# Kernel tuning notes

Measured on AMD Instinct MI355X. Metric: run time of the kernel, lower is better.

## Reference

```python
import jax, jax.numpy as jnp
import numpy as np

B, S, K = 4, 512, 16              # batch, seq_len, random-walk PE length (positional_size)
VOCAB = 50265
D_EMB = 768 - 16 + 16             # 768 - positional_size + extra_positional_size
D_CAT = D_EMB + K                 # 784 = 768 + extra_positional_size


def setup_inputs() -> dict:
    key = jax.random.key(0)
    k0, k1, k2, k3, k4 = jax.random.split(key, 5)
    code_inputs = jax.random.randint(k0, (B, S), 0, VOCAB)
    position_idx = jax.random.randint(k1, (B, S), 0, 8)
    attn_mask = jax.random.randint(k2, (B, S, S), 0, 2).astype(bool)
    emb_table = jax.random.normal(k3, (VOCAB, D_EMB), dtype=jnp.float32) * 0.02
    w_lin = jax.random.normal(k4, (D_CAT, VOCAB), dtype=jnp.float32) * 0.02
    b_lin = jnp.zeros((VOCAB,), dtype=jnp.float32)
    return {"code_inputs": code_inputs, "position_idx": position_idx,
            "attn_mask": attn_mask, "emb_table": emb_table,
            "w_lin": w_lin, "b_lin": b_lin}


def random_walk_pe(attn_mask):
    # adjacency = attn_mask with forced self-loops (adj[:, a, a] = 1)
    eye = jnp.eye(S, dtype=bool)
    A = jnp.where(eye[None], 1.0, attn_mask.astype(jnp.float32))   # [B,S,S]
    deg = A.sum(-1)                                                # out-degree (row sum)
    inv_deg = jnp.where(deg > 0, 1.0 / deg, 0.0)
    M = A * inv_deg[:, :, None]                                    # RW transition D^-1 A

    def step(P, _):
        Pn = jnp.einsum('bij,bjk->bik', P, M)
        return Pn, jnp.diagonal(Pn, axis1=1, axis2=2)              # diag of M^i

    P0 = jnp.broadcast_to(jnp.eye(S, dtype=jnp.float32), (B, S, S))
    _, diags = jax.lax.scan(step, P0, None, length=K)              # [K,B,S]
    return jnp.moveaxis(diags, 0, -1)                              # [B,S,K]


def reference(code_inputs, position_idx, attn_mask, emb_table, w_lin, b_lin):
    nodes_mask = position_idx == 0        # [B,S] DFG nodes
    token_mask = position_idx >= 2        # [B,S] code tokens

    emb = emb_table[code_inputs]          # [B,S,D_EMB]

    # masked average of token embeddings into node positions
    ntm = (nodes_mask[:, :, None] & token_mask[:, None, :] & attn_mask).astype(jnp.float32)
    ntm = ntm / (ntm.sum(-1, keepdims=True) + 1e-10)
    avg = jnp.einsum('abc,acd->abd', ntm, emb)
    emb = jnp.where(nodes_mask[:, :, None], avg, emb)

    pe = random_walk_pe(attn_mask)                    # [B,S,K]
    x = jnp.concatenate([emb, pe], axis=-1)           # [B,S,D_CAT]

    # (external pretrained BERT encoder omitted — identity; see notes)
    logit = jnp.einsum('bsd,dv->bsv', x, w_lin) + b_lin
    return logit
```

## Files before the change

### kernel.cpp

```cpp
#include <hip/hip_runtime.h>

#define VOCAB_N 50265
#define NPAD    50304
#define KX      832
#define DEMB    768
#define DCAT    784
#define SEQ     512
#define NBATCH  4
#define OUT_ROWS 2048
#define PE_ELE  ((size_t)NBATCH*SEQ*SEQ)

typedef unsigned short u16;
typedef unsigned long long u64;
typedef short s16x8 __attribute__((ext_vector_type(8)));
typedef float f32x4 __attribute__((ext_vector_type(4)));
typedef u16   u16x4 __attribute__((ext_vector_type(4)));

#define AS1 __attribute__((address_space(1)))
#define AS3 __attribute__((address_space(3)))

__device__ __forceinline__ u16 f2bf(float f){
  unsigned u = __builtin_bit_cast(unsigned, f);
  u = (u + 0x7FFFu + ((u >> 16) & 1u)) >> 16;
  return (u16)u;
}
__device__ __forceinline__ float bf2f(u16 h){
  return __builtin_bit_cast(float, (unsigned)h << 16);
}
__device__ __forceinline__ void gl_lds16(const void* g, void* l){
  __builtin_amdgcn_global_load_lds((const AS1 unsigned*)g, (AS3 unsigned*)l, 16, 0, 0);
}
__device__ __forceinline__ int xcd_remap(int bid, int nwg){
  int q = nwg >> 3, r = nwg & 7;
  int xc = bid & 7, i = bid >> 3;
  int base = xc < r ? xc*(q+1) : r*(q+1) + (xc - r)*q;
  return base + i;
}

__global__ __launch_bounds__(256) void wconv(const float* __restrict__ w, u16* __restrict__ wT){
  __shared__ float tile[64][65];
  const int n0 = blockIdx.x * 64;
  const int k0 = blockIdx.y * 64;
  const int t = threadIdx.x;
#pragma unroll
  for (int i = 0; i < 16; ++i){
    int idx = t + i*256;
    int kk = idx >> 6, nn = idx & 63;
    int k = k0 + kk, n = n0 + nn;
    float v = 0.f;
    if (k < DCAT && n < VOCAB_N) v = w[(size_t)k*VOCAB_N + n];
    tile[kk][nn] = v;
  }
  __syncthreads();
#pragma unroll
  for (int i = 0; i < 4; ++i){
    int idx = t + i*256;
    int nn = idx >> 4, ks = (idx & 15) * 4;
    u16x4 o;
    o[0] = f2bf(tile[ks+0][nn]);
    o[1] = f2bf(tile[ks+1][nn]);
    o[2] = f2bf(tile[ks+2][nn]);
    o[3] = f2bf(tile[ks+3][nn]);
    *reinterpret_cast<u16x4*>(&wT[(size_t)(n0+nn)*KX + k0 + ks]) = o;
  }
}

__global__ __launch_bounds__(256) void gather_emb(const int* __restrict__ code, const float* __restrict__ emb,
                                                  u16* __restrict__ x){
  const int row = blockIdx.x;
  const int c = code[row];
  const float* e = emb + (size_t)c * DEMB;
  for (int i = threadIdx.x; i < KX; i += 256){
    u16 v = 0;
    if (i < DEMB) v = f2bf(e[i]);
    x[(size_t)row*KX + i] = v;
  }
}

__global__ __launch_bounds__(256) void node_avg(const int* __restrict__ code, const int* __restrict__ pos,
                                                const int* __restrict__ attn, const float* __restrict__ emb,
                                                u16* __restrict__ x){
  const int row = blockIdx.x;
  const int b = row >> 9, i = row & (SEQ-1);
  if (pos[row] != 0) return;
  __shared__ unsigned char sel[SEQ];
  __shared__ int crow[SEQ];
  __shared__ int cnt_s;
  const int t = threadIdx.x;
  if (t == 0) cnt_s = 0;
  __syncthreads();
  int local = 0;
  for (int j = t; j < SEQ; j += 256){
    bool s = (pos[b*SEQ + j] >= 2) && (attn[((size_t)(b*SEQ + i))*SEQ + j] != 0);
    sel[j] = s ? 1 : 0;
    crow[j] = code[b*SEQ + j];
    local += s ? 1 : 0;
  }
  atomicAdd(&cnt_s, local);
  __syncthreads();
  const float scale = 1.0f / ((float)cnt_s + 1e-10f);
  for (int d = t; d < DEMB; d += 256){
    float acc = 0.f;
    for (int j = 0; j < SEQ; ++j){
      if (sel[j]) acc += emb[(size_t)crow[j]*DEMB + d];
    }
    x[(size_t)row*KX + d] = f2bf(acc * scale);
  }
}

__global__ __launch_bounds__(256) void build_M(const int* __restrict__ attn, u16* __restrict__ M,
                                               u16* __restrict__ MT, u16* __restrict__ x){
  const int row = blockIdx.x;
  const int b = row >> 9, i = row & (SEQ-1);
  __shared__ float arow[SEQ];
  __shared__ int deg_s;
  const int t = threadIdx.x;
  if (t == 0) deg_s = 0;
  __syncthreads();
  int local = 0;
  for (int j = t; j < SEQ; j += 256){
    int a = (j == i) ? 1 : ((attn[((size_t)(b*SEQ + i))*SEQ + j] != 0) ? 1 : 0);
    arow[j] = (float)a;
    local += a;
  }
  atomicAdd(&deg_s, local);
  __syncthreads();
  const float inv = 1.0f / (float)deg_s;
  for (int j = t; j < SEQ; j += 256){
    u16 m = f2bf(arow[j] * inv);
    M [((size_t)(b*SEQ + i))*SEQ + j] = m;
    MT[((size_t)(b*SEQ + j))*SEQ + i] = m;
  }
  if (t == 0) x[(size_t)row*KX + DEMB] = f2bf(inv);
}

__global__ __launch_bounds__(256) void pe_pow(const u16* __restrict__ A, const u16* __restrict__ Bn,
                                              u16* __restrict__ C, u16* __restrict__ x, int xcol){
  const int m0 = blockIdx.x * 64, n0 = blockIdx.y * 64, b = blockIdx.z;
  const u16* Ab = A  + (size_t)b*SEQ*SEQ;
  const u16* Bb = Bn + (size_t)b*SEQ*SEQ;
  __shared__ __align__(16) u16 Al[64*64];
  __shared__ __align__(16) u16 Bl[64*64];
  const int t = threadIdx.x, lane = t & 63, w = t >> 6;
  const int wr = w >> 1, wc = w & 1;
  f32x4 acc[2][2] = {};
  const int srow = lane >> 3;
  const int scol = ((lane & 7) ^ srow) * 8;
  for (int k0 = 0; k0 < SEQ; k0 += 64){
    __syncthreads();
#pragma unroll
    for (int c = 0; c < 2; ++c){
      int chunk = w*2 + c;
      int r = chunk*8 + srow;
      gl_lds16(Ab + (size_t)(m0 + r)*SEQ + k0 + scol, Al + chunk*512);
      gl_lds16(Bb + (size_t)(n0 + r)*SEQ + k0 + scol, Bl + chunk*512);
    }
    asm volatile("s_waitcnt vmcnt(0)" ::: "memory");
    __syncthreads();
#pragma unroll
    for (int kin = 0; kin < 2; ++kin){
      s16x8 fa[2], fb[2];
      const int kb = kin*64 + (lane >> 4)*16;
#pragma unroll
      for (int m = 0; m < 2; ++m){
        int r = wr*32 + m*16 + (lane & 15);
        fa[m] = *reinterpret_cast<const s16x8*>((const char*)Al + r*128 + (kb ^ ((r & 7) << 4)));
      }
#pragma unroll
      for (int n = 0; n < 2; ++n){
        int r = wc*32 + n*16 + (lane & 15);
        fb[n] = *reinterpret_cast<const s16x8*>((const char*)Bl + r*128 + (kb ^ ((r & 7) << 4)));
      }
#pragma unroll
      for (int m = 0; m < 2; ++m)
#pragma unroll
        for (int n = 0; n < 2; ++n)
          acc[m][n] = __builtin_amdgcn_mfma_f32_16x16x32_bf16(fa[m], fb[n], acc[m][n], 0, 0, 0);
    }
  }
#pragma unroll
  for (int m = 0; m < 2; ++m)
#pragma unroll
   for (int n = 0; n < 2; ++n)
#pragma unroll
    for (int r = 0; r < 4; ++r){
      int gm = m0 + wr*32 + m*16 + (lane >> 4)*4 + r;
      int gn = n0 + wc*32 + n*16 + (lane & 15);
      u16 bv = f2bf(acc[m][n][r]);
      C[((size_t)(b*SEQ + gm))*SEQ + gn] = bv;
      if (gm == gn) x[(size_t)(b*SEQ + gm)*KX + xcol] = bv;
    }
}

__global__ __launch_bounds__(256) void transpose_k(const u16* __restrict__ in, u16* __restrict__ outp){
  const int i0 = blockIdx.x*64, j0 = blockIdx.y*64, b = blockIdx.z;
  const u16* ib = in   + (size_t)b*SEQ*SEQ;
  u16*       ob = outp + (size_t)b*SEQ*SEQ;
  __shared__ u16 tile[64][66];
  const int t = threadIdx.x;
#pragma unroll
  for (int it = 0; it < 2; ++it){
    int jj = it*32 + (t >> 3), ii = (t & 7)*8;
    s16x8 v = *reinterpret_cast<const s16x8*>(ib + (size_t)(j0+jj)*SEQ + i0 + ii);
#pragma unroll
    for (int q = 0; q < 8; ++q) tile[jj][ii+q] = (u16)v[q];
  }
  __syncthreads();
#pragma unroll
  for (int it = 0; it < 2; ++it){
    int ii = it*32 + (t >> 3), jj8 = (t & 7)*8;
    u16 tmp[8];
#pragma unroll
    for (int q = 0; q < 8; ++q) tmp[q] = tile[jj8+q][ii];
    *reinterpret_cast<s16x8*>(ob + (size_t)(i0+ii)*SEQ + j0 + jj8) = *reinterpret_cast<s16x8*>(tmp);
  }
}

__global__ __launch_bounds__(256) void pe_dots(const u16* __restrict__ M, const u16* __restrict__ pw,
                                               const u16* __restrict__ p8t, u16* __restrict__ x){
  const int row = blockIdx.x;
  const int lane = threadIdx.x & 63, w = threadIdx.x >> 6;
  const u16* t8 = p8t + (size_t)row*SEQ;
  s16x8 vb = *reinterpret_cast<const s16x8*>(t8 + lane*8);
#pragma unroll
  for (int s = 0; s < 2; ++s){
    int a = 1 + w + s*4;
    const u16* Pa = (a == 1) ? (M + (size_t)row*SEQ) : (pw + (size_t)(a-2)*PE_ELE + (size_t)row*SEQ);
    s16x8 va = *reinterpret_cast<const s16x8*>(Pa + lane*8);
    float acc = 0.f;
#pragma unroll
    for (int q = 0; q < 8; ++q) acc += bf2f((u16)va[q]) * bf2f((u16)vb[q]);
#pragma unroll
    for (int m = 32; m; m >>= 1) acc += __shfl_xor(acc, m, 64);
    if (lane == 0) x[(size_t)row*KX + DEMB + 8 + (a-1)] = f2bf(acc);
  }
}

__global__ __launch_bounds__(256) void gemm_fast(const u16* __restrict__ X, const u16* __restrict__ WT,
                                                 const float* __restrict__ bias, float* __restrict__ out,
                                                 int nmt, int nwg){
  const int lid = xcd_remap(blockIdx.x, nwg);
  const int mt = lid % nmt, nt = lid / nmt;
  const int m0 = mt*128, n0 = nt*128;
  __shared__ __align__(16) u16 Al[128*64];
  __shared__ __align__(16) u16 Bl[128*64];
  const int t = threadIdx.x, lane = t & 63, w = t >> 6;
  const int wr = w >> 1, wc = w & 1;
  f32x4 acc[4][4] = {};
  const int srow = lane >> 3;
  const int scol = ((lane & 7) ^ srow) * 8;
  for (int k0 = 0; k0 < KX; k0 += 64){
    __syncthreads();
#pragma unroll
    for (int c = 0; c < 4; ++c){
      int chunk = w*4 + c;
      int r = chunk*8 + srow;
      gl_lds16(X  + (size_t)(m0 + r)*KX + k0 + scol, Al + chunk*512);
      gl_lds16(WT + (size_t)(n0 + r)*KX + k0 + scol, Bl + chunk*512);
    }
    asm volatile("s_waitcnt vmcnt(0)" ::: "memory");
    __syncthreads();
#pragma unroll
    for (int kin = 0; kin < 2; ++kin){
      s16x8 fa[4], fb[4];
      const int kb = kin*64 + (lane >> 4)*16;
#pragma unroll
      for (int m = 0; m < 4; ++m){
        int r = wr*64 + m*16 + (lane & 15);
        fa[m] = *reinterpret_cast<const s16x8*>((const char*)Al + r*128 + (kb ^ ((r & 7) << 4)));
      }
#pragma unroll
      for (int n = 0; n < 4; ++n){
        int r = wc*64 + n*16 + (lane & 15);
        fb[n] = *reinterpret_cast<const s16x8*>((const char*)Bl + r*128 + (kb ^ ((r & 7) << 4)));
      }
#pragma unroll
      for (int m = 0; m < 4; ++m)
#pragma unroll
        for (int n = 0; n < 4; ++n)
          acc[m][n] = __builtin_amdgcn_mfma_f32_16x16x32_bf16(fa[m], fb[n], acc[m][n], 0, 0, 0);
    }
  }
#pragma unroll
  for (int m = 0; m < 4; ++m)
#pragma unroll
   for (int n = 0; n < 4; ++n)
#pragma unroll
    for (int r = 0; r < 4; ++r){
      int gm = m0 + wr*64 + m*16 + (lane >> 4)*4 + r;
      int gn = n0 + wc*64 + n*16 + (lane & 15);
      if (gn < VOCAB_N)
        out[(size_t)gm*VOCAB_N + gn] = acc[m][n][r] + bias[gn];
    }
}

__global__ __launch_bounds__(256) void gemm_slow(const u16* __restrict__ X, const float* __restrict__ W,
                                                 const float* __restrict__ bias, float* __restrict__ out,
                                                 int nwg){
  const int lid = xcd_remap(blockIdx.x, nwg);
  const int mt = 12 + (lid & 3), nt = lid >> 2;
  const int m0 = mt*128, n0 = nt*128;
  __shared__ __align__(16) u16 Al[128*64];
  __shared__ __align__(16) u16 Bl[128*64];
  char* Blc = reinterpret_cast<char*>(Bl);
  const int t = threadIdx.x, lane = t & 63, w = t >> 6;
  const int wr = w >> 1, wc = w & 1;
  f32x4 acc[4][4] = {};
  const int srow = lane >> 3;
  const int scol = ((lane & 7) ^ srow) * 8;
  const int nn  = t & 127;
  const int kk0 = (t >> 7) * 32;
  const int ng  = n0 + nn;
  const bool nok = (ng < VOCAB_N);
  const int bsw = nn*128;
  const int xsw = (nn & 15) << 3;
  for (int k0 = 0; k0 < KX; k0 += 64){
    __syncthreads();
#pragma unroll
    for (int c = 0; c < 4; ++c){
      int chunk = w*4 + c;
      int r = chunk*8 + srow;
      gl_lds16(X + (size_t)(m0 + r)*KX + k0 + scol, Al + chunk*512);
    }
#pragma unroll
    for (int i = 0; i < 16; ++i){
      int k = kk0 + 2*i;
      int gk = k0 + k;
      float f0 = (nok && gk     < DCAT) ? W[(size_t)gk    *VOCAB_N + ng] : 0.f;
      float f1 = (nok && gk + 1 < DCAT) ? W[(size_t)(gk+1)*VOCAB_N + ng] : 0.f;
      unsigned pk = (unsigned)f2bf(f0) | ((unsigned)f2bf(f1) << 16);
      *reinterpret_cast<unsigned*>(Blc + bsw + ((k*2) ^ xsw)) = pk;
    }
    asm volatile("s_waitcnt vmcnt(0)" ::: "memory");
    __syncthreads();
#pragma unroll
    for (int kin = 0; kin < 2; ++kin){
      s16x8 fa[4], fb[4];
      const int kb = kin*64 + (lane >> 4)*16;
#pragma unroll
      for (int m = 0; m < 4; ++m){
        int r = wr*64 + m*16 + (lane & 15);
        fa[m] = *reinterpret_cast<const s16x8*>((const char*)Al + r*128 + (kb ^ ((r & 7) << 4)));
      }
#pragma unroll
      for (int n = 0; n < 4; ++n){
        int row = wc*64 + n*16 + (lane & 15);
        int kbb = kin*64 + (lane >> 4)*16;
        int rsw = (row & 15) << 3;
        u64 h0 = *reinterpret_cast<const u64*>(Blc + row*128 + ((kbb    ) ^ rsw));
        u64 h1 = *reinterpret_cast<const u64*>(Blc + row*128 + ((kbb + 8) ^ rsw));
        struct U128 { u64 a, b; } u{h0, h1};
        fb[n] = __builtin_bit_cast(s16x8, u);
      }
#pragma unroll
      for (int m = 0; m < 4; ++m)
#pragma unroll
        for (int n = 0; n < 4; ++n)
          acc[m][n] = __builtin_amdgcn_mfma_f32_16x16x32_bf16(fa[m], fb[n], acc[m][n], 0, 0, 0);
    }
  }
#pragma unroll
  for (int m = 0; m < 4; ++m)
#pragma unroll
   for (int n = 0; n < 4; ++n)
#pragma unroll
    for (int r = 0; r < 4; ++r){
      int gm = m0 + wr*64 + m*16 + (lane >> 4)*4 + r;
      int gn = n0 + wc*64 + n*16 + (lane & 15);
      if (gn < VOCAB_N)
        out[(size_t)gm*VOCAB_N + gn] = acc[m][n][r] + bias[gn];
    }
}

extern "C" void kernel_launch(void* const* d_in, const int* in_sizes, int n_in,
                              void* d_out, int out_size, void* d_ws, size_t ws_size,
                              hipStream_t stream) {
  (void)in_sizes; (void)n_in; (void)out_size;
  const int*   code = (const int*)d_in[0];
  const int*   pos  = (const int*)d_in[1];
  const int*   attn = (const int*)d_in[2];
  const float* emb  = (const float*)d_in[3];
  const float* wlin = (const float*)d_in[4];
  const float* bias = (const float*)d_in[5];
  float* out = (float*)d_out;

  const size_t WT_ELE  = (size_t)NPAD * KX;
  const size_t X_ELE   = (size_t)OUT_ROWS * KX;
  const size_t OUT_ELE = (size_t)OUT_ROWS * VOCAB_N;
  const size_t need_full = (WT_ELE + X_ELE + 2*PE_ELE + 8*PE_ELE) * sizeof(u16);

  u16 *wT, *x, *M, *MT, *pw, *p8t;
  const bool compact = (ws_size < need_full);
  if (!compact){
    wT  = (u16*)d_ws;
    x   = wT + WT_ELE;
    M   = x  + X_ELE;
    MT  = M  + PE_ELE;
    pw  = MT + PE_ELE;
    p8t = pw + 7*PE_ELE;
  } else {
    x   = (u16*)d_ws;
    M   = x + X_ELE;
    MT  = M + PE_ELE;
    pw  = (u16*)d_out;
    p8t = pw + 7*PE_ELE;
    wT  = (u16*)d_out + (OUT_ELE*2 - WT_ELE);
  }

  wconv     <<<dim3(NPAD/64, KX/64), 256, 0, stream>>>(wlin, wT);
  gather_emb<<<NBATCH*SEQ, 256, 0, stream>>>(code, emb, x);
  node_avg  <<<NBATCH*SEQ, 256, 0, stream>>>(code, pos, attn, emb, x);
  build_M   <<<NBATCH*SEQ, 256, 0, stream>>>(attn, M, MT, x);

  const u16* A = M;
  for (int c = 2; c <= 8; ++c){
    u16* C = pw + (size_t)(c-2)*PE_ELE;
    pe_pow<<<dim3(8,8,NBATCH), 256, 0, stream>>>(A, MT, C, x, DEMB + (c-1));
    A = C;
  }
  transpose_k<<<dim3(8,8,NBATCH), 256, 0, stream>>>(pw + 6*PE_ELE, p8t);
  pe_dots<<<NBATCH*SEQ, 256, 0, stream>>>(M, pw, p8t, x);

  if (!compact){
    const int nwg = (NPAD/128)*16;
    gemm_fast<<<nwg, 256, 0, stream>>>(x, wT, bias, out, 16, nwg);
  } else {
    const int nwg_f = (NPAD/128)*12;
    gemm_fast<<<nwg_f, 256, 0, stream>>>(x, wT, bias, out, 12, nwg_f);
    const int nwg_s = (NPAD/128)*4;
    gemm_slow<<<nwg_s, 256, 0, stream>>>(x, wlin, bias, out, nwg_s);
  }
}
```

Baseline: 1.151 ms.

## Double-buffer LDS in GEMMs, compact node_avg gather list, tiled transpose for MT

The main logits GEMM and the PE power GEMM now use two LDS buffers, so the global-to-LDS loads for the next k tile are issued before the MFMAs on the current tile run, hiding load latency. node_avg builds a compact list of selected token rows with an atomic counter and accumulates them with float4 loads, instead of scanning all 512 positions per column. build_M no longer writes the transpose with strided scattered stores; a tiled transpose kernel produces MT instead. Double buffering doubles LDS use per block, which may lower occupancy, and the atomic list makes the summation order in node_avg nondeterministic.

```diff
diff --git a/kernel.cpp b/kernel.cpp
--- a/kernel.cpp
+++ b/kernel.cpp
@@ -81,39 +81,47 @@
                                                 const int* __restrict__ attn, const float* __restrict__ emb,
                                                 u16* __restrict__ x){
   const int row = blockIdx.x;
-  const int b = row >> 9, i = row & (SEQ-1);
+  const int b = row >> 9;
   if (pos[row] != 0) return;
-  __shared__ unsigned char sel[SEQ];
-  __shared__ int crow[SEQ];
+  __shared__ int list[SEQ];
   __shared__ int cnt_s;
   const int t = threadIdx.x;
   if (t == 0) cnt_s = 0;
   __syncthreads();
-  int local = 0;
   for (int j = t; j < SEQ; j += 256){
-    bool s = (pos[b*SEQ + j] >= 2) && (attn[((size_t)(b*SEQ + i))*SEQ + j] != 0);
-    sel[j] = s ? 1 : 0;
-    crow[j] = code[b*SEQ + j];
-    local += s ? 1 : 0;
-  }
-  atomicAdd(&cnt_s, local);
-  __syncthreads();
-  const float scale = 1.0f / ((float)cnt_s + 1e-10f);
-  for (int d = t; d < DEMB; d += 256){
-    float acc = 0.f;
-    for (int j = 0; j < SEQ; ++j){
-      if (sel[j]) acc += emb[(size_t)crow[j]*DEMB + d];
-    }
-    x[(size_t)row*KX + d] = f2bf(acc * scale);
+    if (pos[b*SEQ + j] >= 2 && attn[(size_t)row*SEQ + j] != 0){
+      int slot = atomicAdd(&cnt_s, 1);
+      list[slot] = code[b*SEQ + j] * DEMB;
+    }
+  }
+  __syncthreads();
+  const int cnt = cnt_s;
+  const float scale = 1.0f / ((float)cnt + 1e-10f);
+  if (t < DEMB/4){
+    f32x4 acc = {};
+    int k = 0;
+    for (; k + 4 <= cnt; k += 4){
+      f32x4 v0 = reinterpret_cast<const f32x4*>(emb + list[k+0])[t];
+      f32x4 v1 = reinterpret_cast<const f32x4*>(emb + list[k+1])[t];
+      f32x4 v2 = reinterpret_cast<const f32x4*>(emb + list[k+2])[t];
+      f32x4 v3 = reinterpret_cast<const f32x4*>(emb + list[k+3])[t];
+      acc += v0; acc += v1; acc += v2; acc += v3;
+    }
+    for (; k < cnt; ++k)
+      acc += reinterpret_cast<const f32x4*>(emb + list[k])[t];
+    u16x4 o;
+#pragma unroll
+    for (int q = 0; q < 4; ++q) o[q] = f2bf(acc[q] * scale);
+    *reinterpret_cast<u16x4*>(&x[(size_t)row*KX + t*4]) = o;
   }
 }
 
 __global__ __launch_bounds__(256) void build_M(const int* __restrict__ attn, u16* __restrict__ M,
-                                               u16* __restrict__ MT, u16* __restrict__ x){
+                                               u16* __restrict__ x){
   const int row = blockIdx.x;
   const int b = row >> 9, i = row & (SEQ-1);
+  __shared__ int deg_s;
   __shared__ float arow[SEQ];
-  __shared__ int deg_s;
   const int t = threadIdx.x;
   if (t == 0) deg_s = 0;
   __syncthreads();
@@ -126,37 +134,59 @@
   atomicAdd(&deg_s, local);
   __syncthreads();
   const float inv = 1.0f / (float)deg_s;
-  for (int j = t; j < SEQ; j += 256){
-    u16 m = f2bf(arow[j] * inv);
-    M [((size_t)(b*SEQ + i))*SEQ + j] = m;
-    MT[((size_t)(b*SEQ + j))*SEQ + i] = m;
-  }
+  for (int j = t; j < SEQ; j += 256)
+    M[((size_t)(b*SEQ + i))*SEQ + j] = f2bf(arow[j] * inv);
   if (t == 0) x[(size_t)row*KX + DEMB] = f2bf(inv);
 }
+
+__global__ __launch_bounds__(256) void transpose_k(const u16* __restrict__ in, u16* __restrict__ outp){
+  const int i0 = blockIdx.x*64, j0 = blockIdx.y*64, b = blockIdx.z;
+  const u16* ib = in   + (size_t)b*SEQ*SEQ;
+  u16*       ob = outp + (size_t)b*SEQ*SEQ;
+  __shared__ u16 tile[64][66];
+  const int t = threadIdx.x;
+#pragma unroll
+  for (int it = 0; it < 2; ++it){
+    int jj = it*32 + (t >> 3), ii = (t & 7)*8;
+    s16x8 v = *reinterpret_cast<const s16x8*>(ib + (size_t)(j0+jj)*SEQ + i0 + ii);
+#pragma unroll
+    for (int q = 0; q < 8; ++q) tile[jj][ii+q] = (u16)v[q];
+  }
+  __syncthreads();
+#pragma unroll
+  for (int it = 0; it < 2; ++it){
+    int ii = it*32 + (t >> 3), jj8 = (t & 7)*8;
+    u16 tmp[8];
+#pragma unroll
+    for (int q = 0; q < 8; ++q) tmp[q] = tile[jj8+q][ii];
+    *reinterpret_cast<s16x8*>(ob + (size_t)(i0+ii)*SEQ + j0 + jj8) = *reinterpret_cast<s16x8*>(tmp);
+  }
+}
+
+#define PP_STAGE(kt, bf) do{ const int _k0 = (kt)*64;                              \
+  for (int _c = 0; _c < 2; ++_c){                                                  \
+    int _ch = w*2 + _c; int _r = _ch*8 + srow;                                     \
+    gl_lds16(Ab + (size_t)(m0 + _r)*SEQ + _k0 + scol, &Al[bf][_ch*512]);           \
+    gl_lds16(Bb + (size_t)(n0 + _r)*SEQ + _k0 + scol, &Bl[bf][_ch*512]); } }while(0)
 
 __global__ __launch_bounds__(256) void pe_pow(const u16* __restrict__ A, const u16* __restrict__ Bn,
                                               u16* __restrict__ C, u16* __restrict__ x, int xcol){
   const int m0 = blockIdx.x * 64, n0 = blockIdx.y * 64, b = blockIdx.z;
   const u16* Ab = A  + (size_t)b*SEQ*SEQ;
   const u16* Bb = Bn + (size_t)b*SEQ*SEQ;
-  __shared__ __align__(16) u16 Al[64*64];
-  __shared__ __align__(16) u16 Bl[64*64];
+  __shared__ __align__(16) u16 Al[2][64*64];
+  __shared__ __align__(16) u16 Bl[2][64*64];
   const int t = threadIdx.x, lane = t & 63, w = t >> 6;
   const int wr = w >> 1, wc = w & 1;
   f32x4 acc[2][2] = {};
   const int srow = lane >> 3;
   const int scol = ((lane & 7) ^ srow) * 8;
-  for (int k0 = 0; k0 < SEQ; k0 += 64){
-    __syncthreads();
-#pragma unroll
-    for (int c = 0; c < 2; ++c){
-      int chunk = w*2 + c;
-      int r = chunk*8 + srow;
-      gl_lds16(Ab + (size_t)(m0 + r)*SEQ + k0 + scol, Al + chunk*512);
-      gl_lds16(Bb + (size_t)(n0 + r)*SEQ + k0 + scol, Bl + chunk*512);
-    }
-    asm volatile("s_waitcnt vmcnt(0)" ::: "memory");
-    __syncthreads();
+  PP_STAGE(0, 0);
+  asm volatile("s_waitcnt vmcnt(0)" ::: "memory");
+  __syncthreads();
+  for (int kt = 0; kt < SEQ/64; ++kt){
+    const int cur = kt & 1;
+    if (kt + 1 < SEQ/64) PP_STAGE(kt+1, cur^1);
 #pragma unroll
     for (int kin = 0; kin < 2; ++kin){
       s16x8 fa[2], fb[2];
@@ -164,12 +194,12 @@
 #pragma unroll
       for (int m = 0; m < 2; ++m){
         int r = wr*32 + m*16 + (lane & 15);
-        fa[m] = *reinterpret_cast<const s16x8*>((const char*)Al + r*128 + (kb ^ ((r & 7) << 4)));
+        fa[m] = *reinterpret_cast<const s16x8*>((const char*)&Al[cur][0] + r*128 + (kb ^ ((r & 7) << 4)));
       }
 #pragma unroll
       for (int n = 0; n < 2; ++n){
         int r = wc*32 + n*16 + (lane & 15);
-        fb[n] = *reinterpret_cast<const s16x8*>((const char*)Bl + r*128 + (kb ^ ((r & 7) << 4)));
+        fb[n] = *reinterpret_cast<const s16x8*>((const char*)&Bl[cur][0] + r*128 + (kb ^ ((r & 7) << 4)));
       }
 #pragma unroll
       for (int m = 0; m < 2; ++m)
@@ -177,6 +207,8 @@
         for (int n = 0; n < 2; ++n)
           acc[m][n] = __builtin_amdgcn_mfma_f32_16x16x32_bf16(fa[m], fb[n], acc[m][n], 0, 0, 0);
     }
+    asm volatile("s_waitcnt vmcnt(0)" ::: "memory");
+    __syncthreads();
   }
 #pragma unroll
   for (int m = 0; m < 2; ++m)
@@ -192,30 +224,6 @@
     }
 }
 
-__global__ __launch_bounds__(256) void transpose_k(const u16* __restrict__ in, u16* __restrict__ outp){
-  const int i0 = blockIdx.x*64, j0 = blockIdx.y*64, b = blockIdx.z;
-  const u16* ib = in   + (size_t)b*SEQ*SEQ;
-  u16*       ob = outp + (size_t)b*SEQ*SEQ;
-  __shared__ u16 tile[64][66];
-  const int t = threadIdx.x;
-#pragma unroll
-  for (int it = 0; it < 2; ++it){
-    int jj = it*32 + (t >> 3), ii = (t & 7)*8;
-    s16x8 v = *reinterpret_cast<const s16x8*>(ib + (size_t)(j0+jj)*SEQ + i0 + ii);
-#pragma unroll
-    for (int q = 0; q < 8; ++q) tile[jj][ii+q] = (u16)v[q];
-  }
-  __syncthreads();
-#pragma unroll
-  for (int it = 0; it < 2; ++it){
-    int ii = it*32 + (t >> 3), jj8 = (t & 7)*8;
-    u16 tmp[8];
-#pragma unroll
-    for (int q = 0; q < 8; ++q) tmp[q] = tile[jj8+q][ii];
-    *reinterpret_cast<s16x8*>(ob + (size_t)(i0+ii)*SEQ + j0 + jj8) = *reinterpret_cast<s16x8*>(tmp);
-  }
-}
-
 __global__ __launch_bounds__(256) void pe_dots(const u16* __restrict__ M, const u16* __restrict__ pw,
                                                const u16* __restrict__ p8t, u16* __restrict__ x){
   const int row = blockIdx.x;
@@ -236,30 +244,32 @@
   }
 }
 
+#define GF_STAGE(kt, bf) do{ const int _k0 = (kt)*64;                              \
+  for (int _c = 0; _c < 4; ++_c){                                                  \
+    int _ch = w*4 + _c; int _r = _ch*8 + srow;                                     \
+    gl_lds16(X  + (size_t)(m0 + _r)*KX + _k0 + scol, &Al[bf][_ch*512]);            \
+    gl_lds16(WT + (size_t)(n0 + _r)*KX + _k0 + scol, &Bl[bf][_ch*512]); } }while(0)
+
 __global__ __launch_bounds__(256) void gemm_fast(const u16* __restrict__ X, const u16* __restrict__ WT,
                                                  const float* __restrict__ bias, float* __restrict__ out,
                                                  int nmt, int nwg){
   const int lid = xcd_remap(blockIdx.x, nwg);
   const int mt = lid % nmt, nt = lid / nmt;
   const int m0 = mt*128, n0 = nt*128;
-  __shared__ __align__(16) u16 Al[128*64];
-  __shared__ __align__(16) u16 Bl[128*64];
+  __shared__ __align__(16) u16 Al[2][128*64];
+  __shared__ __align__(16) u16 Bl[2][128*64];
   const int t = threadIdx.x, lane = t & 63, w = t >> 6;
   const int wr = w >> 1, wc = w & 1;
   f32x4 acc[4][4] = {};
   const int srow = lane >> 3;
   const int scol = ((lane & 7) ^ srow) * 8;
-  for (int k0 = 0; k0 < KX; k0 += 64){
-    __syncthreads();
-#pragma unroll
-    for (int c = 0; c < 4; ++c){
-      int chunk = w*4 + c;
-      int r = chunk*8 + srow;
-      gl_lds16(X  + (size_t)(m0 + r)*KX + k0 + scol, Al + chunk*512);
-      gl_lds16(WT + (size_t)(n0 + r)*KX + k0 + scol, Bl + chunk*512);
-    }
-    asm volatile("s_waitcnt vmcnt(0)" ::: "memory");
-    __syncthreads();
+  GF_STAGE(0, 0);
+  asm volatile("s_waitcnt vmcnt(0)" ::: "memory");
+  __syncthreads();
+  const int NKT = KX/64;
+  for (int kt = 0; kt < NKT; ++kt){
+    const int cur = kt & 1;
+    if (kt + 1 < NKT) GF_STAGE(kt+1, cur^1);
 #pragma unroll
     for (int kin = 0; kin < 2; ++kin){
       s16x8 fa[4], fb[4];
@@ -267,12 +277,12 @@
 #pragma unroll
       for (int m = 0; m < 4; ++m){
         int r = wr*64 + m*16 + (lane & 15);
-        fa[m] = *reinterpret_cast<const s16x8*>((const char*)Al + r*128 + (kb ^ ((r & 7) << 4)));
+        fa[m] = *reinterpret_cast<const s16x8*>((const char*)&Al[cur][0] + r*128 + (kb ^ ((r & 7) << 4)));
       }
 #pragma unroll
       for (int n = 0; n < 4; ++n){
         int r = wc*64 + n*16 + (lane & 15);
-        fb[n] = *reinterpret_cast<const s16x8*>((const char*)Bl + r*128 + (kb ^ ((r & 7) << 4)));
+        fb[n] = *reinterpret_cast<const s16x8*>((const char*)&Bl[cur][0] + r*128 + (kb ^ ((r & 7) << 4)));
       }
 #pragma unroll
       for (int m = 0; m < 4; ++m)
@@ -280,6 +290,8 @@
         for (int n = 0; n < 4; ++n)
           acc[m][n] = __builtin_amdgcn_mfma_f32_16x16x32_bf16(fa[m], fb[n], acc[m][n], 0, 0, 0);
     }
+    asm volatile("s_waitcnt vmcnt(0)" ::: "memory");
+    __syncthreads();
   }
 #pragma unroll
   for (int m = 0; m < 4; ++m)
@@ -316,7 +328,6 @@
   const int xsw = (nn & 15) << 3;
   for (int k0 = 0; k0 < KX; k0 += 64){
     __syncthreads();
-#pragma unroll
     for (int c = 0; c < 4; ++c){
       int chunk = w*4 + c;
       int r = chunk*8 + srow;
@@ -407,10 +418,11 @@
     wT  = (u16*)d_out + (OUT_ELE*2 - WT_ELE);
   }
 
-  wconv     <<<dim3(NPAD/64, KX/64), 256, 0, stream>>>(wlin, wT);
-  gather_emb<<<NBATCH*SEQ, 256, 0, stream>>>(code, emb, x);
-  node_avg  <<<NBATCH*SEQ, 256, 0, stream>>>(code, pos, attn, emb, x);
-  build_M   <<<NBATCH*SEQ, 256, 0, stream>>>(attn, M, MT, x);
+  wconv      <<<dim3(NPAD/64, KX/64), 256, 0, stream>>>(wlin, wT);
+  gather_emb <<<NBATCH*SEQ, 256, 0, stream>>>(code, emb, x);
+  node_avg   <<<NBATCH*SEQ, 256, 0, stream>>>(code, pos, attn, emb, x);
+  build_M    <<<NBATCH*SEQ, 256, 0, stream>>>(attn, M, x);
+  transpose_k<<<dim3(8,8,NBATCH), 256, 0, stream>>>(M, MT);
 
   const u16* A = M;
   for (int c = 2; c <= 8; ++c){
```

After: 1.001 ms. 13.0% less time.
